# Kernel tuning notes

Measured on AMD Instinct MI355X. Metric: run time of the kernel, lower is better.

## Reference

```python
import jax, jax.numpy as jnp
import numpy as np

B, T, C, L = 32, 800, 5000, 100  # batch, frames, vocab(incl blank=0), max label len
NEG = -1e30  # log-zero surrogate (safe for logsumexp, avoids inf-inf NaNs)


def setup_inputs() -> dict:
    key = jax.random.key(0)
    k1, k2_, k3, k4 = jax.random.split(key, 4)
    # nnet_output is assumed to be log-softmax output of the acoustic model
    nnet_output = jax.nn.log_softmax(jax.random.normal(k1, (B, T, C), jnp.float32), axis=-1)
    targets = jax.random.randint(k2_, (B, L), 1, C).astype(jnp.int32)  # labels in [1, C)
    input_lengths = (T - jax.random.randint(k3, (B,), 0, T // 4)).astype(jnp.int32)
    target_lengths = (L - jax.random.randint(k4, (B,), 0, L // 4)).astype(jnp.int32)
    return dict(nnet_output=nnet_output, targets=targets,
                input_lengths=input_lengths, target_lengths=target_lengths)


def _ctc_tot_scores(log_probs, targets, input_lengths, target_lengths):
    """Log-semiring total score of the CTC numerator lattice per utterance.
    Equivalent to k2.intersect_dense(num_graphs, dense_fsa_vec).get_tot_scores(log_semiring=True).
    """
    Bb, Tt, Cc = log_probs.shape
    Ll = targets.shape[1]
    S = 2 * Ll + 1  # extended label sequence with interleaved blanks
    ext = jnp.zeros((Bb, S), targets.dtype).at[:, 1::2].set(targets)  # [B,S]
    # emission scores gathered along the extended labels: [B,T,S]
    emit = jnp.take_along_axis(log_probs, jnp.broadcast_to(ext[:, None, :], (Bb, Tt, S)), axis=2)
    emit_seq = jnp.transpose(emit, (1, 0, 2))  # [T,B,S]
    # skip transition s-2 -> s allowed iff ext[s] != blank and ext[s] != ext[s-2]
    ext_m2 = jnp.pad(ext[:, :-2], ((0, 0), (2, 0)), constant_values=-1)
    skip_ok = (ext != 0) & (ext != ext_m2)  # [B,S]

    alpha0 = jnp.full((Bb, S), NEG, log_probs.dtype)
    alpha0 = alpha0.at[:, 0].set(emit_seq[0, :, 0]).at[:, 1].set(emit_seq[0, :, 1])

    def step(alpha, emit_t):
        a1 = alpha
        a2 = jnp.pad(alpha[:, :-1], ((0, 0), (1, 0)), constant_values=NEG)
        a3 = jnp.where(skip_ok, jnp.pad(alpha[:, :-2], ((0, 0), (2, 0)), constant_values=NEG), NEG)
        m = jnp.maximum(jnp.maximum(a1, a2), a3)
        new = m + jnp.log(jnp.exp(a1 - m) + jnp.exp(a2 - m) + jnp.exp(a3 - m)) + emit_t
        return new, new

    _, alphas_rest = jax.lax.scan(step, alpha0, emit_seq[1:])
    alphas = jnp.concatenate([alpha0[None], alphas_rest], axis=0)  # [T,B,S]

    bidx = jnp.arange(Bb)
    final_alpha = alphas[input_lengths - 1, bidx, :]  # [B,S] alpha at last valid frame
    s_last = 2 * target_lengths       # final blank state
    s_prev = 2 * target_lengths - 1   # final label state
    tot = jnp.logaddexp(final_alpha[bidx, s_last], final_alpha[bidx, s_prev])  # [B]
    return tot


def reference(nnet_output, targets, input_lengths, target_lengths):
    tot_scores = _ctc_tot_scores(nnet_output, targets, input_lengths, target_lengths)
    finite = tot_scores > (NEG / 2)  # mirrors get_tot_objf_and_num_frames filtering -inf
    frames = input_lengths.astype(jnp.int64)
    tot_score = jnp.sum(jnp.where(finite, tot_scores, 0.0))
    tot_frames = jnp.sum(jnp.where(finite, frames, 0))
    all_frames = jnp.sum(frames)
    return (tot_score, tot_frames, all_frames)
```

## Files before the change

kernel.cpp:

```cpp
#include <hip/hip_runtime.h>


constexpr int B  = 32;
constexpr int T  = 800;
constexpr int C  = 5000;
constexpr int L  = 100;
constexpr int S  = 2 * L + 1;
constexpr float NEGV = -1e30f;

constexpr int RP  = 104;
constexpr int CH  = 64;
constexpr int CHE = CH * RP;
constexpr int BLK = 320;
constexpr int NPROD = 256;
constexpr int GCH = 32;
constexpr size_t WS_NEED = (size_t)B * T * RP * sizeof(float);

__device__ __forceinline__ float lse2(float a, float b) {
    const float m = fmaxf(a, b);
    return m + __logf(__expf(a - m) + __expf(b - m));
}
__device__ __forceinline__ float lse3(float a, float b, float c) {
    const float m = fmaxf(a, fmaxf(b, c));
    return m + __logf(__expf(a - m) + __expf(b - m) + __expf(c - m));
}

__global__ __launch_bounds__(128) void ctc_gather(
    const float* __restrict__ lp, const int* __restrict__ targets,
    const int* __restrict__ il_, float* __restrict__ ws)
{
    __shared__ int tgt[L];
    const int b  = blockIdx.x;
    const int t0 = blockIdx.y * GCH;
    const int j  = threadIdx.x;
    if (j < L) tgt[j] = targets[b * L + j];
    __syncthreads();

    const int il   = il_[b];
    const int rows = ((il - t0) < GCH) ? (il - t0) : GCH;
    if (rows <= 0 || j >= RP) return;

    float* __restrict__ dst = ws + ((size_t)b * T + t0) * RP + j;

    if (j > 100) {
#pragma unroll
        for (int i = 0; i < GCH; ++i)
            if (i < rows) dst[(size_t)i * RP] = NEGV;
        return;
    }
    const int cls = (j < 100) ? tgt[j] : 0;
    const float* __restrict__ sp = lp + ((size_t)b * T + t0) * C + cls;

    if (rows == GCH) {
#pragma unroll 8
        for (int i = 0; i < GCH; ++i)
            dst[(size_t)i * RP] = sp[(size_t)i * C];
    } else {
        for (int i = 0; i < rows; ++i)
            dst[(size_t)i * RP] = sp[(size_t)i * C];
    }
}

__global__ __launch_bounds__(BLK) void ctc_alpha(
    const float* __restrict__ ws, const int* __restrict__ targets,
    const int* __restrict__ il_, const int* __restrict__ tl_,
    float* __restrict__ out)
{
    __shared__ float buf[2][CHE];
    __shared__ int   tgt[L];
    __shared__ float sm[256];

    const int b   = blockIdx.x;
    const int tid = threadIdx.x;
    const int il  = il_[b];
    const int nch = (il + CH - 1) / CH;
    const float* __restrict__ base = ws + (size_t)b * T * RP;

    if (tid < L) tgt[tid] = targets[b * L + tid];
    __syncthreads();

    const int lane = tid;
    const int s0   = 4 * lane;
    bool skip1 = false, skip3 = false;
    bool v0 = false, v1 = false, v2c = false, v3 = false;
    int  offt = 0;
    if (tid < 64) {
        const int l2 = 2 * lane;
        const int i1 = (l2     < L) ? l2     : L - 1;
        const int i3 = (l2 + 1 < L) ? l2 + 1 : L - 1;
        const int ip = (l2 - 1 >= 0) ? l2 - 1 : 0;
        const int c1i = tgt[i1], c3i = tgt[i3], cpi = tgt[ip];
        skip1 = (lane == 0) ? true : (c1i != cpi);
        skip3 = (c3i != c1i);
        v0  = (s0     < S);
        v1  = (s0 + 1 < S);
        v2c = (s0 + 2 < S);
        v3  = (s0 + 3 < S);
        offt = (l2 <= 100) ? l2 : 100;
    }

    float a0 = NEGV, a1v = NEGV, a2v = NEGV, a3v = NEGV;

    for (int c = -1; c < nch; ++c) {
        if (tid >= 64) {
            const int c2 = c + 1;
            if (c2 < nch) {
                const int rows = ((il - c2 * CH) < CH) ? (il - c2 * CH) : CH;
                const int jmax = rows * (RP / 4);
                float4* __restrict__ dst = (float4*)buf[c2 & 1];
                const float4* __restrict__ src =
                    (const float4*)(base + (size_t)c2 * CHE);
                for (int j = tid - 64; j < jmax; j += NPROD) dst[j] = src[j];
            }
        } else if (c >= 0) {
            const float* bp = buf[c & 1];
            const int tbase = c * CH;
            const int rmax  = (il - tbase < CH) ? (il - tbase) : CH;
            float2 tv = *(const float2*)(bp + offt);
            float  bl = bp[100];
            for (int r = 0; r < rmax; ++r) {
                const float2 ctv = tv;
                const float  cbl = bl;
                if (r + 1 < rmax) {
                    tv = *(const float2*)(bp + (r + 1) * RP + offt);
                    bl = bp[(r + 1) * RP + 100];
                }
                const int t = tbase + r;
                if (t == 0) {
                    a0  = (lane == 0) ? cbl   : NEGV;
                    a1v = (lane == 0) ? ctv.x : NEGV;
                    a2v = NEGV; a3v = NEGV;
                } else {
                    float up3 = __shfl_up(a3v, 1);
                    if (lane == 0) up3 = NEGV;
                    const float n0 = lse2(a0, up3) + cbl;
                    const float n1 = (skip1 ? lse3(a1v, a0, up3) : lse2(a1v, a0)) + ctv.x;
                    const float n2 = lse2(a2v, a1v) + cbl;
                    const float n3 = (skip3 ? lse3(a3v, a2v, a1v) : lse2(a3v, a2v)) + ctv.y;
                    a0  = v0  ? n0 : NEGV;
                    a1v = v1  ? n1 : NEGV;
                    a2v = v2c ? n2 : NEGV;
                    a3v = v3  ? n3 : NEGV;
                }
            }
        }
        __syncthreads();
    }

    if (tid < 64) {
        sm[s0 + 0] = a0;
        sm[s0 + 1] = a1v;
        sm[s0 + 2] = a2v;
        sm[s0 + 3] = a3v;
    }
    __syncthreads();

    if (tid == 0) {
        const int tl = tl_[b];
        const float tot = lse2(sm[2 * tl], sm[2 * tl - 1]);
        const bool finite = tot > (NEGV * 0.5f);
        atomicAdd(out + 0, finite ? tot : 0.0f);
        atomicAdd(out + 1, finite ? (float)il : 0.0f);
        atomicAdd(out + 2, (float)il);
    }
}

constexpr int SPF  = 204;
constexpr int CHF  = 32;
constexpr int CHEF = CHF * SPF;

__global__ __launch_bounds__(BLK) void ctc_fused(
    const float* __restrict__ lp, const int* __restrict__ targets,
    const int* __restrict__ il_, const int* __restrict__ tl_,
    float* __restrict__ out)
{
    __shared__ float buf[2][CHEF];
    __shared__ int   tgt[L];
    __shared__ float sm[256];

    const int b   = blockIdx.x;
    const int tid = threadIdx.x;
    const int il  = il_[b];
    const int nch = (il + CHF - 1) / CHF;
    const float* __restrict__ base = lp + (size_t)b * T * C;

    if (tid < L) tgt[tid] = targets[b * L + tid];
    __syncthreads();

    const int lane = tid;
    const int s0   = 4 * lane;
    bool skip1 = false, skip3 = false;
    bool v0 = false, v1 = false, v2c = false, v3 = false;
    int  off = 0;
    if (tid < 64) {
        const int l2 = 2 * lane;
        const int i1 = (l2     < L) ? l2     : L - 1;
        const int i3 = (l2 + 1 < L) ? l2 + 1 : L - 1;
        const int ip = (l2 - 1 >= 0) ? l2 - 1 : 0;
        const int c1i = tgt[i1], c3i = tgt[i3], cpi = tgt[ip];
        skip1 = (lane == 0) ? true : (c1i != cpi);
        skip3 = (c3i != c1i);
        v0  = (s0     < S);
        v1  = (s0 + 1 < S);
        v2c = (s0 + 2 < S);
        v3  = (s0 + 3 < S);
        off = (s0 <= 200) ? s0 : 200;
    }

    float a0 = NEGV, a1v = NEGV, a2v = NEGV, a3v = NEGV;

    for (int c = -1; c < nch; ++c) {
        if (tid >= 64) {
            const int c2 = c + 1;
            if (c2 < nch) {
                float* dst = buf[c2 & 1];
                const int tbase = c2 * CHF;
                const int pid = tid - 64;
#pragma unroll
                for (int bat = 0; bat < 2; ++bat) {
                    float v[13];
                    int   fl[13];
#pragma unroll
                    for (int j = 0; j < 13; ++j) {
                        const int flat = (bat * 13 + j) * NPROD + pid;
                        fl[j] = flat;
                        float val = NEGV;
                        if (flat < CHEF) {
                            const int r = flat / SPF;
                            const int s = flat - r * SPF;
                            const int t = tbase + r;
                            if (t < il) {
                                const int cls = ((s & 1) && s < S) ? tgt[s >> 1] : 0;
                                val = base[(size_t)t * C + cls];
                            }
                        }
                        v[j] = val;
                    }
#pragma unroll
                    for (int j = 0; j < 13; ++j)
                        if (fl[j] < CHEF) dst[fl[j]] = v[j];
                }
            }
        } else if (c >= 0) {
            const float* bp = buf[c & 1];
            const int tbase = c * CHF;
            const int rmax  = (il - tbase < CHF) ? (il - tbase) : CHF;
            float4 e = *(const float4*)(bp + off);
            for (int r = 0; r < rmax; ++r) {
                const float4 cur = e;
                if (r + 1 < rmax) e = *(const float4*)(bp + (r + 1) * SPF + off);
                const int t = tbase + r;
                if (t == 0) {
                    a0  = (lane == 0) ? cur.x : NEGV;
                    a1v = (lane == 0) ? cur.y : NEGV;
                    a2v = NEGV; a3v = NEGV;
                } else {
                    float up3 = __shfl_up(a3v, 1);
                    if (lane == 0) up3 = NEGV;
                    const float n0 = lse2(a0, up3) + cur.x;
                    const float n1 = (skip1 ? lse3(a1v, a0, up3) : lse2(a1v, a0)) + cur.y;
                    const float n2 = lse2(a2v, a1v) + cur.z;
                    const float n3 = (skip3 ? lse3(a3v, a2v, a1v) : lse2(a3v, a2v)) + cur.w;
                    a0  = v0  ? n0 : NEGV;
                    a1v = v1  ? n1 : NEGV;
                    a2v = v2c ? n2 : NEGV;
                    a3v = v3  ? n3 : NEGV;
                }
            }
        }
        __syncthreads();
    }

    if (tid < 64) {
        sm[s0 + 0] = a0;
        sm[s0 + 1] = a1v;
        sm[s0 + 2] = a2v;
        sm[s0 + 3] = a3v;
    }
    __syncthreads();

    if (tid == 0) {
        const int tl = tl_[b];
        const float tot = lse2(sm[2 * tl], sm[2 * tl - 1]);
        const bool finite = tot > (NEGV * 0.5f);
        atomicAdd(out + 0, finite ? tot : 0.0f);
        atomicAdd(out + 1, finite ? (float)il : 0.0f);
        atomicAdd(out + 2, (float)il);
    }
}

extern "C" void kernel_launch(void* const* d_in, const int* in_sizes, int n_in,
                              void* d_out, int out_size, void* d_ws, size_t ws_size,
                              hipStream_t stream)
{
    const float* lp      = (const float*)d_in[0];
    const int*   targets = (const int*)d_in[1];
    const int*   il      = (const int*)d_in[2];
    const int*   tl      = (const int*)d_in[3];
    float* out = (float*)d_out;

    hipMemsetAsync(d_out, 0, (size_t)out_size * sizeof(float), stream);

    if (ws_size >= WS_NEED) {
        float* ws = (float*)d_ws;
        ctc_gather<<<dim3(B, T / GCH), 128, 0, stream>>>(lp, targets, il, ws);
        ctc_alpha<<<B, BLK, 0, stream>>>(ws, targets, il, tl, out);
    } else {
        ctc_fused<<<B, BLK, 0, stream>>>(lp, targets, il, tl, out);
    }
}
```

Baseline: 884.2 us.

## Fuse gather and alpha into one persistent kernel with flag-based producer/consumer pipelining

Replaces the separate gather and alpha kernels with one launch. Extra blocks gather emissions chunk by chunk and publish per-chunk ready flags, and the alpha blocks spin on those flags. The gather blocks now stream whole log-prob rows into shared memory with coalesced float4 loads and pick the target columns from there, instead of strided scalar global reads. The aim is to overlap the gather with the serial alpha recursion and improve read coalescing. In exchange it reads full rows, roughly 20KB per frame, so more bytes move, and it depends on all blocks being co-resident to avoid deadlock. It also adds a flag memset.

Result: slower. 1.045 ms (+18.2%).

```diff
diff --git a/kernel.cpp b/kernel.cpp
--- a/kernel.cpp
+++ b/kernel.cpp
@@ -11,10 +11,19 @@
 constexpr int RP  = 104;
 constexpr int CH  = 64;
 constexpr int CHE = CH * RP;
+constexpr int NCHUNK = (T + CH - 1) / CH;
+constexpr int T_PAD  = NCHUNK * CH;
+constexpr int NT  = NCHUNK * B;
 constexpr int BLK = 320;
-constexpr int NPROD = 256;
-constexpr int GCH = 32;
-constexpr size_t WS_NEED = (size_t)B * T * RP * sizeof(float);
+constexpr int NALPHA  = B;
+constexpr int NGATHER = 224;
+constexpr int NBLOCKS = NALPHA + NGATHER;
+constexpr int ROWV4   = C / 4;
+
+constexpr size_t DATA_FLOATS = (size_t)B * T_PAD * RP;
+constexpr size_t WS_NEED = (DATA_FLOATS + NT) * sizeof(float);
+
+constexpr int ARENA_BYTES = 2 * CHE * 4 + L * 4 + 256 * 4;
 
 __device__ __forceinline__ float lse2(float a, float b) {
     const float m = fmaxf(a, b);
@@ -25,56 +34,72 @@
     return m + __logf(__expf(a - m) + __expf(b - m) + __expf(c - m));
 }
 
-__global__ __launch_bounds__(128) void ctc_gather(
+__global__ __launch_bounds__(BLK) void ctc_pipe(
     const float* __restrict__ lp, const int* __restrict__ targets,
-    const int* __restrict__ il_, float* __restrict__ ws)
+    const int* __restrict__ il_, const int* __restrict__ tl_,
+    float* __restrict__ out, float* __restrict__ ws, int* __restrict__ flags)
 {
-    __shared__ int tgt[L];
-    const int b  = blockIdx.x;
-    const int t0 = blockIdx.y * GCH;
-    const int j  = threadIdx.x;
-    if (j < L) tgt[j] = targets[b * L + j];
-    __syncthreads();
-
-    const int il   = il_[b];
-    const int rows = ((il - t0) < GCH) ? (il - t0) : GCH;
-    if (rows <= 0 || j >= RP) return;
-
-    float* __restrict__ dst = ws + ((size_t)b * T + t0) * RP + j;
-
-    if (j > 100) {
-#pragma unroll
-        for (int i = 0; i < GCH; ++i)
-            if (i < rows) dst[(size_t)i * RP] = NEGV;
+    alignas(16) __shared__ char arena[ARENA_BYTES];
+    const int bid = blockIdx.x;
+    const int tid = threadIdx.x;
+
+    if (bid >= NALPHA) {
+        float* rowbuf = (float*)arena;
+        int*   tgt    = (int*)(arena + 2 * C * 4);
+        const int gb = bid - NALPHA;
+
+        for (int task = gb; task < NT; task += NGATHER) {
+            const int b     = task & 31;
+            const int chunk = task >> 5;
+            const int t0    = chunk * CH;
+            const int il    = il_[b];
+            int rows = il - t0; rows = rows > CH ? CH : rows;
+
+            if (rows > 0) {
+                if (tid < L) tgt[tid] = targets[b * L + tid];
+                const float* __restrict__ src = lp + (size_t)(b * T + t0) * C;
+                float* __restrict__ dstb = ws + ((size_t)b * T_PAD + t0) * RP;
+                {
+                    const float4* s4 = (const float4*)src;
+                    float4* d4 = (float4*)rowbuf;
+                    for (int j = tid; j < ROWV4; j += BLK) d4[j] = s4[j];
+                }
+                __syncthreads();
+                for (int r = 0; r < rows; ++r) {
+                    if (r + 1 < rows) {
+                        const float4* s4 = (const float4*)(src + (size_t)(r + 1) * C);
+                        float4* d4 = (float4*)(rowbuf + ((r + 1) & 1) * C);
+                        for (int j = tid; j < ROWV4; j += BLK) d4[j] = s4[j];
+                    }
+                    const float* rb = rowbuf + (r & 1) * C;
+                    if (tid < RP) {
+                        float v;
+                        if      (tid < 100)  v = rb[tgt[tid]];
+                        else if (tid == 100) v = rb[0];
+                        else                 v = NEGV;
+                        dstb[(size_t)r * RP + tid] = v;
+                    }
+                    __syncthreads();
+                }
+            }
+            __threadfence();
+            if (tid == 0)
+                __hip_atomic_store(flags + task, 1, __ATOMIC_RELEASE,
+                                   __HIP_MEMORY_SCOPE_AGENT);
+            __syncthreads();
+        }
         return;
     }
-    const int cls = (j < 100) ? tgt[j] : 0;
-    const float* __restrict__ sp = lp + ((size_t)b * T + t0) * C + cls;
-
-    if (rows == GCH) {
-#pragma unroll 8
-        for (int i = 0; i < GCH; ++i)
-            dst[(size_t)i * RP] = sp[(size_t)i * C];
-    } else {
-        for (int i = 0; i < rows; ++i)
-            dst[(size_t)i * RP] = sp[(size_t)i * C];
-    }
-}
-
-__global__ __launch_bounds__(BLK) void ctc_alpha(
-    const float* __restrict__ ws, const int* __restrict__ targets,
-    const int* __restrict__ il_, const int* __restrict__ tl_,
-    float* __restrict__ out)
-{
-    __shared__ float buf[2][CHE];
-    __shared__ int   tgt[L];
-    __shared__ float sm[256];
-
-    const int b   = blockIdx.x;
-    const int tid = threadIdx.x;
-    const int il  = il_[b];
+
+    float* buf0 = (float*)arena;
+    float* buf1 = (float*)(arena + CHE * 4);
+    int*   tgt  = (int*)(arena + 2 * CHE * 4);
+    float* sm   = (float*)(arena + 2 * CHE * 4 + L * 4);
+
+    const int b  = bid;
+    const int il = il_[b];
     const int nch = (il + CH - 1) / CH;
-    const float* __restrict__ base = ws + (size_t)b * T * RP;
+    const float* __restrict__ base = ws + (size_t)b * T_PAD * RP;
 
     if (tid < L) tgt[tid] = targets[b * L + tid];
     __syncthreads();
@@ -105,15 +130,20 @@
         if (tid >= 64) {
             const int c2 = c + 1;
             if (c2 < nch) {
+                const int task = (c2 << 5) + b;
+                while (__hip_atomic_load(flags + task, __ATOMIC_ACQUIRE,
+                                         __HIP_MEMORY_SCOPE_AGENT) == 0) {
+                    __builtin_amdgcn_s_sleep(2);
+                }
                 const int rows = ((il - c2 * CH) < CH) ? (il - c2 * CH) : CH;
                 const int jmax = rows * (RP / 4);
-                float4* __restrict__ dst = (float4*)buf[c2 & 1];
+                float4* __restrict__ dst = (float4*)((c2 & 1) ? buf1 : buf0);
                 const float4* __restrict__ src =
                     (const float4*)(base + (size_t)c2 * CHE);
-                for (int j = tid - 64; j < jmax; j += NPROD) dst[j] = src[j];
+                for (int j = tid - 64; j < jmax; j += 256) dst[j] = src[j];
             }
         } else if (c >= 0) {
-            const float* bp = buf[c & 1];
+            const float* bp = (c & 1) ? buf1 : buf0;
             const int tbase = c * CH;
             const int rmax  = (il - tbase < CH) ? (il - tbase) : CH;
             float2 tv = *(const float2*)(bp + offt);
@@ -168,6 +198,7 @@
 constexpr int SPF  = 204;
 constexpr int CHF  = 32;
 constexpr int CHEF = CHF * SPF;
+constexpr int NPROD = 256;
 
 __global__ __launch_bounds__(BLK) void ctc_fused(
     const float* __restrict__ lp, const int* __restrict__ targets,
@@ -302,9 +333,10 @@
     hipMemsetAsync(d_out, 0, (size_t)out_size * sizeof(float), stream);
 
     if (ws_size >= WS_NEED) {
-        float* ws = (float*)d_ws;
-        ctc_gather<<<dim3(B, T / GCH), 128, 0, stream>>>(lp, targets, il, ws);
-        ctc_alpha<<<B, BLK, 0, stream>>>(ws, targets, il, tl, out);
+        float* ws   = (float*)d_ws;
+        int*  flags = (int*)(ws + DATA_FLOATS);
+        hipMemsetAsync(flags, 0, NT * sizeof(int), stream);
+        ctc_pipe<<<NBLOCKS, BLK, 0, stream>>>(lp, targets, il, tl, out, ws, flags);
     } else {
         ctc_fused<<<B, BLK, 0, stream>>>(lp, targets, il, tl, out);
     }
```
